# Kernel optimization log

Measured on AMD Instinct MI355X. Metric: run time of the kernel, lower is better.

The kernel has to match this reference:

```python
import jax, jax.numpy as jnp
import numpy as np

B, S, D = 2, 2048, 1024
E, K, DFF = 8, 2, 4 * 1024
EPS_GATE = 1e-8
EPS_LN = 1e-5


def setup_inputs() -> dict:
    key = jax.random.key(0)
    ks = jax.random.split(key, 4)
    scaled = lambda k, shape, fan: (jax.random.normal(k, shape, jnp.float32) / np.sqrt(fan).astype(np.float32))
    return {
        "x": jax.random.normal(ks[0], (B, S, D), jnp.float32),
        "Wg": scaled(ks[1], (D, E), D),
        "bg": jnp.zeros((E,), jnp.float32),
        "W1": scaled(ks[2], (E, D, DFF), D),
        "b1": jnp.zeros((E, DFF), jnp.float32),
        "W2": scaled(ks[3], (E, DFF, D), DFF),
        "b2": jnp.zeros((E, D), jnp.float32),
        "gamma": jnp.ones((D,), jnp.float32),
        "beta": jnp.zeros((D,), jnp.float32),
    }


def reference(x, Wg, bg, W1, b1, W2, b2, gamma, beta):
    b, s, d = x.shape
    xf = x.reshape(-1, d)                       # [T, D]
    T = xf.shape[0]
    num_experts = Wg.shape[1]

    # Gating: softmax over experts, top-k, renormalize selected weights.
    logits = xf @ Wg + bg                       # [T, E]
    w = jax.nn.softmax(logits, axis=-1)
    top_w, top_idx = jax.lax.top_k(w, K)        # [T, K]
    top_w = top_w / (top_w.sum(axis=-1, keepdims=True) + EPS_GATE)

    # Dense combine weights: cw[t, e] = renormalized weight if e selected else 0.
    cw = jnp.zeros((T, num_experts), xf.dtype).at[
        jnp.arange(T)[:, None], top_idx].add(top_w)

    # Expert FFNs (loop over small fixed expert count), weighted combine.
    out = jnp.zeros_like(xf)
    for e in range(num_experts):
        h = jax.nn.gelu(xf @ W1[e] + b1[e], approximate=False)  # [T, DFF]
        y = h @ W2[e] + b2[e]                                    # [T, D]
        out = out + cw[:, e:e + 1] * y

    # LayerNorm over the whole combined output (as in the torch module).
    mu = out.mean(axis=-1, keepdims=True)
    var = out.var(axis=-1, keepdims=True)
    out = (out - mu) / jnp.sqrt(var + EPS_LN) * gamma + beta
    return out.reshape(b, s, d)
```

## Files before the change

### kernel.cpp

```cpp
#include <hip/hip_runtime.h>
#include <hip/hip_bf16.h>

#define TOK  4096
#define DIMD 1024
#define NEXP 8
#define DFFN 4096
#define NSLOT   (TOK*2 + NEXP*128)
#define NRB128  ((TOK*2)/128 + NEXP)

typedef __attribute__((ext_vector_type(8))) short bf16x8;
typedef __attribute__((ext_vector_type(4))) float f32x4;

__device__ __forceinline__ unsigned short f2bf(float f){
  unsigned int u = __float_as_uint(f);
  unsigned int r = u + 0x7FFFu + ((u >> 16) & 1u);
  return (unsigned short)(r >> 16);
}

__device__ __forceinline__ float bf2f(unsigned short h){
  unsigned int u = ((unsigned int)h) << 16;
  return __uint_as_float(u);
}

__device__ __forceinline__ void gload_lds16(const void* g, void* l){
  __builtin_amdgcn_global_load_lds(
      (const __attribute__((address_space(1))) unsigned int*)g,
      (__attribute__((address_space(3))) unsigned int*)l, 16, 0, 0);
}

__global__ __launch_bounds__(256) void k_gate_trw1(
    const float* __restrict__ x, const float* __restrict__ Wg,
    const float* __restrict__ bg, int* __restrict__ topidx,
    float* __restrict__ topw, int* __restrict__ pos, int* __restrict__ count,
    unsigned short* __restrict__ xb,
    const float* __restrict__ W1, unsigned short* __restrict__ w1t)
{
  if (blockIdx.x < 2048){
    const int bid = blockIdx.x;
    const int e = bid >> 8, rem = bid & 255;
    const int R = DIMD, C = DFFN;
    const float* I = W1 + (size_t)e * R * C;
    unsigned short* O = w1t + (size_t)e * R * C;
    const int r0 = (rem >> 5) * 128, c0 = (rem & 31) * 128;
    __shared__ alignas(16) unsigned short tile[128*128];
    const int tid = threadIdx.x;
    const int qw = tid & 31;
    const int rw = tid >> 5;
    #pragma unroll
    for (int it = 0; it < 16; ++it){
      const int r = it * 8 + rw;
      const float4 v = *(const float4*)(I + (size_t)(r0 + r) * C + c0 + qw * 4);
      ushort4 o;
      o.x = f2bf(v.x); o.y = f2bf(v.y); o.z = f2bf(v.z); o.w = f2bf(v.w);
      const int slot = qw ^ ((r >> 2) & 31);
      *(ushort4*)&tile[r * 128 + slot * 4] = o;
    }
    __syncthreads();
    const int p  = tid & 31;
    const int cb = tid >> 5;
    #pragma unroll
    for (int it = 0; it < 4; ++it){
      const int cg = cb * 4 + it;
      const int sl = (cg ^ p) * 4;
      const ushort4 a0 = *(const ushort4*)&tile[(4*p + 0) * 128 + sl];
      const ushort4 a1 = *(const ushort4*)&tile[(4*p + 1) * 128 + sl];
      const ushort4 a2 = *(const ushort4*)&tile[(4*p + 2) * 128 + sl];
      const ushort4 a3 = *(const ushort4*)&tile[(4*p + 3) * 128 + sl];
      ushort4 o;
      o.x = a0.x; o.y = a1.x; o.z = a2.x; o.w = a3.x;
      *(ushort4*)(O + (size_t)(c0 + 4*cg + 0) * R + r0 + 4*p) = o;
      o.x = a0.y; o.y = a1.y; o.z = a2.y; o.w = a3.y;
      *(ushort4*)(O + (size_t)(c0 + 4*cg + 1) * R + r0 + 4*p) = o;
      o.x = a0.z; o.y = a1.z; o.z = a2.z; o.w = a3.z;
      *(ushort4*)(O + (size_t)(c0 + 4*cg + 2) * R + r0 + 4*p) = o;
      o.x = a0.w; o.y = a1.w; o.z = a2.w; o.w = a3.w;
      *(ushort4*)(O + (size_t)(c0 + 4*cg + 3) * R + r0 + 4*p) = o;
    }
    return;
  }
  const int gb = blockIdx.x - 2048;
  const int wid = threadIdx.x >> 6, lane = threadIdx.x & 63;
  const int t = gb * 4 + wid;
  const float* xr = x + (size_t)t * DIMD;
  unsigned short* xbr = xb + (size_t)t * DIMD;
  float acc[NEXP] = {0.f,0.f,0.f,0.f,0.f,0.f,0.f,0.f};
  #pragma unroll
  for (int j = 0; j < DIMD/64; ++j){
    const int d = j*64 + lane;
    const float xv = xr[d];
    xbr[d] = f2bf(xv);
    const float4 wa = *(const float4*)(Wg + (size_t)d*NEXP);
    const float4 wb = *(const float4*)(Wg + (size_t)d*NEXP + 4);
    acc[0] += xv*wa.x; acc[1] += xv*wa.y; acc[2] += xv*wa.z; acc[3] += xv*wa.w;
    acc[4] += xv*wb.x; acc[5] += xv*wb.y; acc[6] += xv*wb.z; acc[7] += xv*wb.w;
  }
  #pragma unroll
  for (int e = 0; e < NEXP; ++e){
    float v = acc[e];
    #pragma unroll
    for (int o = 32; o > 0; o >>= 1) v += __shfl_xor(v, o);
    acc[e] = v;
  }
  if (lane == 0){
    float lg[NEXP], m = -1e30f;
    #pragma unroll
    for (int e = 0; e < NEXP; ++e){ lg[e] = acc[e] + bg[e]; m = fmaxf(m, lg[e]); }
    float p[NEXP], S = 0.f;
    #pragma unroll
    for (int e = 0; e < NEXP; ++e){ p[e] = expf(lg[e] - m); S += p[e]; }
    int e0 = 0;
    #pragma unroll
    for (int e = 1; e < NEXP; ++e) if (p[e] > p[e0]) e0 = e;
    int e1 = (e0 == 0) ? 1 : 0;
    #pragma unroll
    for (int e = 0; e < NEXP; ++e){
      if (e == e0 || e == e1) continue;
      if (p[e] > p[e1]) e1 = e;
    }
    const float denom = p[e0] + p[e1] + 1e-8f * S;
    const float w0 = p[e0] / denom, w1 = p[e1] / denom;
    const int p0 = atomicAdd(&count[e0], 1);
    const int p1 = atomicAdd(&count[e1], 1);
    topidx[t*2] = e0; topidx[t*2+1] = e1;
    topw[t*2] = w0;   topw[t*2+1] = w1;
    pos[t*2] = p0;    pos[t*2+1] = p1;
  }
}

__global__ __launch_bounds__(256) void k_scatter(
    const int* __restrict__ topidx, const int* __restrict__ pos,
    const int* __restrict__ count, int* __restrict__ slot_of, int* __restrict__ tok_of)
{
  int basee[NEXP]; int bacc = 0;
  #pragma unroll
  for (int q = 0; q < NEXP; ++q){
    basee[q] = bacc << 7;
    bacc += (count[q] + 127) >> 7;
  }
  const int t = blockIdx.x * 256 + threadIdx.x;
  #pragma unroll
  for (int k = 0; k < 2; ++k){
    const int e = topidx[t*2+k];
    const int g = basee[e] + pos[t*2+k];
    slot_of[t*2+k] = g;
    tok_of[g] = t;
  }
}

template<int KD, int KSLICES, int NT, int MODE, int WAVES, int BM, int BN, int MINW, int TRW2>
__global__ __launch_bounds__(WAVES*64, MINW) void k_gemm(
    const unsigned short* __restrict__ A, const unsigned short* __restrict__ Bt,
    const float* __restrict__ bias, const int* __restrict__ tok_of,
    const int* __restrict__ count,
    unsigned short* __restrict__ outH, unsigned short* __restrict__ outY,
    unsigned short* __restrict__ outY1,
    const float* __restrict__ W2src, unsigned short* __restrict__ w2tdst)
{
  __shared__ alignas(16) unsigned short smem[BM*64 + BN*64];
  constexpr int CT = NT / BN;

  int by, ct, ks;
  if constexpr (TRW2 != 0){
    by = blockIdx.y;
    if (by >= NRB128){
      const int bid = (by - NRB128) * gridDim.x + blockIdx.x;
      const int eT = bid >> 8, rem = bid & 255;
      const int R = DFFN, C = DIMD;
      const float* I = W2src + (size_t)eT * R * C;
      unsigned short* O = w2tdst + (size_t)eT * R * C;
      const int r0 = (rem >> 3) * 128, c0 = (rem & 7) * 128;
      unsigned short* tile = smem;
      const int tid = threadIdx.x;
      const int qw = tid & 31, rw = tid >> 5;
      #pragma unroll
      for (int it = 0; it < 8; ++it){
        const int r = it * 16 + rw;
        const float4 v = *(const float4*)(I + (size_t)(r0 + r) * C + c0 + qw * 4);
        ushort4 o;
        o.x = f2bf(v.x); o.y = f2bf(v.y); o.z = f2bf(v.z); o.w = f2bf(v.w);
        const int slot = qw ^ ((r >> 2) & 31);
        *(ushort4*)&tile[r * 128 + slot * 4] = o;
      }
      __syncthreads();
      const int p = tid & 31, cb = tid >> 5;
      #pragma unroll
      for (int it = 0; it < 2; ++it){
        const int cg = cb * 2 + it;
        const int sl = (cg ^ p) * 4;
        const ushort4 a0 = *(const ushort4*)&tile[(4*p + 0) * 128 + sl];
        const ushort4 a1 = *(const ushort4*)&tile[(4*p + 1) * 128 + sl];
        const ushort4 a2 = *(const ushort4*)&tile[(4*p + 2) * 128 + sl];
        const ushort4 a3 = *(const ushort4*)&tile[(4*p + 3) * 128 + sl];
        ushort4 o;
        o.x = a0.x; o.y = a1.x; o.z = a2.x; o.w = a3.x;
        *(ushort4*)(O + (size_t)(c0 + 4*cg + 0) * R + r0 + 4*p) = o;
        o.x = a0.y; o.y = a1.y; o.z = a2.y; o.w = a3.y;
        *(ushort4*)(O + (size_t)(c0 + 4*cg + 1) * R + r0 + 4*p) = o;
        o.x = a0.z; o.y = a1.z; o.z = a2.z; o.w = a3.z;
        *(ushort4*)(O + (size_t)(c0 + 4*cg + 2) * R + r0 + 4*p) = o;
        o.x = a0.w; o.y = a1.w; o.z = a2.w; o.w = a3.w;
        *(ushort4*)(O + (size_t)(c0 + 4*cg + 3) * R + r0 + 4*p) = o;
      }
      return;
    }
    const int g = blockIdx.x + (int)gridDim.x * by;
    by = 9 * (g & 7) + ((g % 72) >> 3);
    ct = g / 72;
    ks = 0;
  } else {
    static_assert(CT * KSLICES == 8, "GEMM2 map assumes 8 blocks per rowblock");
    const int g = blockIdx.x;
    const int xx = g & 7;
    const int w  = g >> 3;
    by = 9 * xx + (w % 9);
    const int cw = w / 9;
    ct = cw % CT;
    ks = cw / CT;
  }

  int e = -1, b0 = 0;
  #pragma unroll
  for (int q = 0; q < NEXP; ++q){
    const int nb = (count[q] + 127) >> 7;
    if (e < 0){ if (by < b0 + nb) e = q; else b0 += nb; }
  }
  if (e < 0) return;
  constexpr int KSL = KD / KSLICES;
  const int kbase = ks * KSL;
  const int row0 = by * 128;
  constexpr int T   = WAVES * 64;
  constexpr int RA  = BM*8 / T;
  constexpr int RB  = BN*8 / T;
  constexpr int WN  = BN / 64;
  constexpr int WM  = WAVES / WN;
  constexpr int MR  = BM / WM / 16;
  unsigned short* sA = smem;
  unsigned short* sB = smem + BM*64;
  const int tid = threadIdx.x, wid = tid >> 6, lane = tid & 63;

  const unsigned short* aptr[RA];
  #pragma unroll
  for (int i = 0; i < RA; ++i){
    const int s = i*T + tid;
    const int row = s >> 3;
    const int c = (s & 7) ^ (row & 7);
    size_t arow;
    if (MODE == 1) arow = (size_t)tok_of[row0 + row] * KD;
    else           arow = (size_t)(row0 + row) * KD;
    aptr[i] = A + arow + kbase + c*8;
  }
  const unsigned short* bptr[RB];
  #pragma unroll
  for (int i = 0; i < RB; ++i){
    const int s = i*T + tid;
    const int row = s >> 3;
    const int c = (s & 7) ^ (row & 7);
    bptr[i] = Bt + ((size_t)e*NT + ct*BN + row) * KD + kbase + c*8;
  }

  f32x4 acc[MR][4] = {};
  const int wr = wid / WN, wc = wid % WN;

  int aoff[MR][2], boff[4][2];
  #pragma unroll
  for (int m = 0; m < MR; ++m){
    #pragma unroll
    for (int s = 0; s < 2; ++s){
      const int rowA = wr*(MR*16) + m*16 + (lane & 15);
      aoff[m][s] = rowA*64 + (((s*4) + (lane >> 4)) ^ (rowA & 7))*8;
    }
  }
  #pragma unroll
  for (int n = 0; n < 4; ++n){
    #pragma unroll
    for (int s = 0; s < 2; ++s){
      const int rowB = wc*64 + n*16 + (lane & 15);
      boff[n][s] = rowB*64 + (((s*4) + (lane >> 4)) ^ (rowB & 7))*8;
    }
  }

  for (int k0 = 0; k0 < KSL; k0 += 64){
    #pragma unroll
    for (int i = 0; i < RA; ++i)
      gload_lds16(aptr[i] + k0, &sA[(i*T + tid - lane)*8]);
    #pragma unroll
    for (int i = 0; i < RB; ++i)
      gload_lds16(bptr[i] + k0, &sB[(i*T + tid - lane)*8]);
    __syncthreads();
    #pragma unroll
    for (int s = 0; s < 2; ++s){
      bf16x8 af[MR], bfr[4];
      #pragma unroll
      for (int m = 0; m < MR; ++m) af[m] = *(const bf16x8*)&sA[aoff[m][s]];
      #pragma unroll
      for (int n = 0; n < 4; ++n) bfr[n] = *(const bf16x8*)&sB[boff[n][s]];
      #pragma unroll
      for (int m = 0; m < MR; ++m)
        #pragma unroll
        for (int n = 0; n < 4; ++n)
          acc[m][n] = __builtin_amdgcn_mfma_f32_16x16x32_bf16(af[m], bfr[n], acc[m][n], 0, 0, 0);
    }
    __syncthreads();
  }

  const float* be = bias + (size_t)e * NT;
  unsigned short* outYs = (ks == 0) ? outY : outY1;
  #pragma unroll
  for (int m = 0; m < MR; ++m){
    #pragma unroll
    for (int n = 0; n < 4; ++n){
      #pragma unroll
      for (int j = 0; j < 4; ++j){
        const int rl = wr*(MR*16) + m*16 + ((lane >> 4) << 2) + j;
        const int ng = ct*BN + wc*64 + n*16 + (lane & 15);
        const size_t orow = (size_t)(row0 + rl) * NT + ng;
        if (MODE == 1){
          const float u = acc[m][n][j] + be[ng];
          float y = 0.7978845608028654f * (u + 0.044715f * u * u * u);
          y = fminf(fmaxf(y, -15.f), 15.f);
          const float ex = __expf(2.f * y);
          const float th = (ex - 1.f) / (ex + 1.f);
          outH[orow] = f2bf(0.5f * u * (1.f + th));
        } else {
          outYs[orow] = f2bf(acc[m][n][j] + ((ks == 0) ? be[ng] : 0.f));
        }
      }
    }
  }
}

__global__ __launch_bounds__(256) void k_combine_ln(
    const unsigned short* __restrict__ Ys0, const unsigned short* __restrict__ Ys1,
    const int* __restrict__ slot_of,
    const float* __restrict__ topw, const float* __restrict__ gamma,
    const float* __restrict__ beta, float* __restrict__ out)
{
  const int t = blockIdx.x;
  const int g0 = slot_of[t*2], g1 = slot_of[t*2+1];
  const float w0 = topw[t*2], w1 = topw[t*2+1];
  const int c = threadIdx.x;
  const ushort4 a0 = *(const ushort4*)(Ys0 + (size_t)g0*DIMD + c*4);
  const ushort4 a1 = *(const ushort4*)(Ys1 + (size_t)g0*DIMD + c*4);
  const ushort4 b0 = *(const ushort4*)(Ys0 + (size_t)g1*DIMD + c*4);
  const ushort4 b1 = *(const ushort4*)(Ys1 + (size_t)g1*DIMD + c*4);
  float4 v;
  v.x = w0*(bf2f(a0.x)+bf2f(a1.x)) + w1*(bf2f(b0.x)+bf2f(b1.x));
  v.y = w0*(bf2f(a0.y)+bf2f(a1.y)) + w1*(bf2f(b0.y)+bf2f(b1.y));
  v.z = w0*(bf2f(a0.z)+bf2f(a1.z)) + w1*(bf2f(b0.z)+bf2f(b1.z));
  v.w = w0*(bf2f(a0.w)+bf2f(a1.w)) + w1*(bf2f(b0.w)+bf2f(b1.w));
  float s  = v.x + v.y + v.z + v.w;
  float ss = v.x*v.x + v.y*v.y + v.z*v.z + v.w*v.w;
  #pragma unroll
  for (int o = 32; o > 0; o >>= 1){ s += __shfl_xor(s, o); ss += __shfl_xor(ss, o); }
  __shared__ float red[8];
  const int wid = threadIdx.x >> 6, lane = threadIdx.x & 63;
  if (lane == 0){ red[wid] = s; red[4 + wid] = ss; }
  __syncthreads();
  const float S  = red[0] + red[1] + red[2] + red[3];
  const float SS = red[4] + red[5] + red[6] + red[7];
  const float mu  = S * (1.f/DIMD);
  const float var = SS * (1.f/DIMD) - mu*mu;
  const float inv = rsqrtf(var + 1e-5f);
  const float4 gm = *(const float4*)(gamma + c*4);
  const float4 bt = *(const float4*)(beta + c*4);
  float4 o;
  o.x = (v.x - mu)*inv*gm.x + bt.x;
  o.y = (v.y - mu)*inv*gm.y + bt.y;
  o.z = (v.z - mu)*inv*gm.z + bt.z;
  o.w = (v.w - mu)*inv*gm.w + bt.w;
  *(float4*)(out + (size_t)t*DIMD + c*4) = o;
}

extern "C" void kernel_launch(void* const* d_in, const int* in_sizes, int n_in,
                              void* d_out, int out_size, void* d_ws, size_t ws_size,
                              hipStream_t stream)
{
  const float* x     = (const float*)d_in[0];
  const float* Wg    = (const float*)d_in[1];
  const float* bg    = (const float*)d_in[2];
  const float* W1    = (const float*)d_in[3];
  const float* b1    = (const float*)d_in[4];
  const float* W2    = (const float*)d_in[5];
  const float* b2    = (const float*)d_in[6];
  const float* gamma = (const float*)d_in[7];
  const float* beta  = (const float*)d_in[8];
  float* out = (float*)d_out;

  char* ws = (char*)d_ws;
  size_t off = 0;
  auto alloc = [&](size_t b){ char* p = ws + off; off += (b + 255) & ~(size_t)255; return p; };
  unsigned short* xb  = (unsigned short*)alloc((size_t)TOK*DIMD*2);
  unsigned short* w1t = (unsigned short*)alloc((size_t)NEXP*DFFN*DIMD*2);
  unsigned short* w2t = (unsigned short*)alloc((size_t)NEXP*DIMD*DFFN*2);
  unsigned short* Hs  = (unsigned short*)alloc((size_t)NSLOT*DFFN*2);
  int*   topidx  = (int*)alloc(TOK*2*4);
  float* topw    = (float*)alloc(TOK*2*4);
  int*   pos     = (int*)alloc(TOK*2*4);
  int*   slot_of = (int*)alloc(TOK*2*4);
  int*   tok_of  = (int*)alloc(NSLOT*4);
  int*   count   = (int*)alloc(256);
  unsigned short* Ys0b = (unsigned short*)w1t;
  unsigned short* Ys1b = Ys0b + (size_t)NSLOT*DIMD;

  (void)hipMemsetAsync(count, 0, NEXP*sizeof(int), stream);
  (void)hipMemsetAsync(tok_of, 0, NSLOT*sizeof(int), stream);
  k_gate_trw1<<<3072, 256, 0, stream>>>(x, Wg, bg, topidx, topw, pos, count, xb, W1, w1t);
  k_scatter<<<TOK/256, 256, 0, stream>>>(topidx, pos, count, slot_of, tok_of);
  k_gemm<DIMD, 1, DFFN, 1, 8, 128, 256, 4, 1><<<dim3(DFFN/256, NRB128 + 128), 512, 0, stream>>>(
      xb, w1t, b1, tok_of, count, Hs, nullptr, nullptr, W2, w2t);
  k_gemm<DFFN, 2, DIMD, 2, 8, 128, 256, 4, 0><<<dim3((DIMD/256)*NRB128*2), 512, 0, stream>>>(
      Hs, w2t, b2, tok_of, count, nullptr, Ys0b, Ys1b, nullptr, nullptr);
  k_combine_ln<<<TOK, 256, 0, stream>>>(Ys0b, Ys1b, slot_of, topw, gamma, beta, out);
}
```

Measured before the change: 394.5 us.

## Fuse W1 fp32-to-bf16 conversion into first expert GEMM B-tile load

```diff
diff --git a/kernel.cpp b/kernel.cpp
--- a/kernel.cpp
+++ b/kernel.cpp
@@ -28,57 +28,13 @@
       (__attribute__((address_space(3))) unsigned int*)l, 16, 0, 0);
 }
 
-__global__ __launch_bounds__(256) void k_gate_trw1(
+__global__ __launch_bounds__(256) void k_gate(
     const float* __restrict__ x, const float* __restrict__ Wg,
     const float* __restrict__ bg, int* __restrict__ topidx,
     float* __restrict__ topw, int* __restrict__ pos, int* __restrict__ count,
-    unsigned short* __restrict__ xb,
-    const float* __restrict__ W1, unsigned short* __restrict__ w1t)
-{
-  if (blockIdx.x < 2048){
-    const int bid = blockIdx.x;
-    const int e = bid >> 8, rem = bid & 255;
-    const int R = DIMD, C = DFFN;
-    const float* I = W1 + (size_t)e * R * C;
-    unsigned short* O = w1t + (size_t)e * R * C;
-    const int r0 = (rem >> 5) * 128, c0 = (rem & 31) * 128;
-    __shared__ alignas(16) unsigned short tile[128*128];
-    const int tid = threadIdx.x;
-    const int qw = tid & 31;
-    const int rw = tid >> 5;
-    #pragma unroll
-    for (int it = 0; it < 16; ++it){
-      const int r = it * 8 + rw;
-      const float4 v = *(const float4*)(I + (size_t)(r0 + r) * C + c0 + qw * 4);
-      ushort4 o;
-      o.x = f2bf(v.x); o.y = f2bf(v.y); o.z = f2bf(v.z); o.w = f2bf(v.w);
-      const int slot = qw ^ ((r >> 2) & 31);
-      *(ushort4*)&tile[r * 128 + slot * 4] = o;
-    }
-    __syncthreads();
-    const int p  = tid & 31;
-    const int cb = tid >> 5;
-    #pragma unroll
-    for (int it = 0; it < 4; ++it){
-      const int cg = cb * 4 + it;
-      const int sl = (cg ^ p) * 4;
-      const ushort4 a0 = *(const ushort4*)&tile[(4*p + 0) * 128 + sl];
-      const ushort4 a1 = *(const ushort4*)&tile[(4*p + 1) * 128 + sl];
-      const ushort4 a2 = *(const ushort4*)&tile[(4*p + 2) * 128 + sl];
-      const ushort4 a3 = *(const ushort4*)&tile[(4*p + 3) * 128 + sl];
-      ushort4 o;
-      o.x = a0.x; o.y = a1.x; o.z = a2.x; o.w = a3.x;
-      *(ushort4*)(O + (size_t)(c0 + 4*cg + 0) * R + r0 + 4*p) = o;
-      o.x = a0.y; o.y = a1.y; o.z = a2.y; o.w = a3.y;
-      *(ushort4*)(O + (size_t)(c0 + 4*cg + 1) * R + r0 + 4*p) = o;
-      o.x = a0.z; o.y = a1.z; o.z = a2.z; o.w = a3.z;
-      *(ushort4*)(O + (size_t)(c0 + 4*cg + 2) * R + r0 + 4*p) = o;
-      o.x = a0.w; o.y = a1.w; o.z = a2.w; o.w = a3.w;
-      *(ushort4*)(O + (size_t)(c0 + 4*cg + 3) * R + r0 + 4*p) = o;
-    }
-    return;
-  }
-  const int gb = blockIdx.x - 2048;
+    unsigned short* __restrict__ xb)
+{
+  const int gb = blockIdx.x;
   const int wid = threadIdx.x >> 6, lane = threadIdx.x & 63;
   const int t = gb * 4 + wid;
   const float* xr = x + (size_t)t * DIMD;
@@ -147,14 +103,16 @@
   }
 }
 
-template<int KD, int KSLICES, int NT, int MODE, int WAVES, int BM, int BN, int MINW, int TRW2>
+template<int KD, int KSLICES, int NT, int MODE, int WAVES, int BM, int BN, int MINW,
+         int TRW2, int BF32>
 __global__ __launch_bounds__(WAVES*64, MINW) void k_gemm(
     const unsigned short* __restrict__ A, const unsigned short* __restrict__ Bt,
     const float* __restrict__ bias, const int* __restrict__ tok_of,
     const int* __restrict__ count,
     unsigned short* __restrict__ outH, unsigned short* __restrict__ outY,
     unsigned short* __restrict__ outY1,
-    const float* __restrict__ W2src, unsigned short* __restrict__ w2tdst)
+    const float* __restrict__ W2src, unsigned short* __restrict__ w2tdst,
+    const float* __restrict__ Bf32)
 {
   __shared__ alignas(16) unsigned short smem[BM*64 + BN*64];
   constexpr int CT = NT / BN;
@@ -250,13 +208,18 @@
     aptr[i] = A + arow + kbase + c*8;
   }
   const unsigned short* bptr[RB];
-  #pragma unroll
-  for (int i = 0; i < RB; ++i){
-    const int s = i*T + tid;
-    const int row = s >> 3;
-    const int c = (s & 7) ^ (row & 7);
-    bptr[i] = Bt + ((size_t)e*NT + ct*BN + row) * KD + kbase + c*8;
-  }
+  if constexpr (BF32 == 0){
+    #pragma unroll
+    for (int i = 0; i < RB; ++i){
+      const int s = i*T + tid;
+      const int row = s >> 3;
+      const int c = (s & 7) ^ (row & 7);
+      bptr[i] = Bt + ((size_t)e*NT + ct*BN + row) * KD + kbase + c*8;
+    }
+  }
+  const float* bfp = nullptr;
+  if constexpr (BF32 != 0)
+    bfp = Bf32 + ((size_t)e*KD + kbase + 8*wid) * NT + ct*BN + 4*lane;
 
   f32x4 acc[MR][4] = {};
   const int wr = wid / WN, wc = wid % WN;
@@ -280,12 +243,31 @@
   }
 
   for (int k0 = 0; k0 < KSL; k0 += 64){
-    #pragma unroll
-    for (int i = 0; i < RA; ++i)
-      gload_lds16(aptr[i] + k0, &sA[(i*T + tid - lane)*8]);
-    #pragma unroll
-    for (int i = 0; i < RB; ++i)
-      gload_lds16(bptr[i] + k0, &sB[(i*T + tid - lane)*8]);
+    if constexpr (BF32 != 0){
+      float4 bv[8];
+      const float* bp = bfp + (size_t)k0 * NT;
+      #pragma unroll
+      for (int r = 0; r < 8; ++r) bv[r] = *(const float4*)(bp + (size_t)r * NT);
+      #pragma unroll
+      for (int i = 0; i < RA; ++i)
+        gload_lds16(aptr[i] + k0, &sA[(i*T + tid - lane)*8]);
+      #pragma unroll
+      for (int j = 0; j < 4; ++j){
+        bf16x8 col;
+        #pragma unroll
+        for (int r = 0; r < 8; ++r)
+          col[r] = (short)f2bf(((const float*)&bv[r])[j]);
+        const int n = 4*lane + j;
+        *(bf16x8*)&sB[n*64 + ((wid ^ (n & 7)))*8] = col;
+      }
+    } else {
+      #pragma unroll
+      for (int i = 0; i < RA; ++i)
+        gload_lds16(aptr[i] + k0, &sA[(i*T + tid - lane)*8]);
+      #pragma unroll
+      for (int i = 0; i < RB; ++i)
+        gload_lds16(bptr[i] + k0, &sB[(i*T + tid - lane)*8]);
+    }
     __syncthreads();
     #pragma unroll
     for (int s = 0; s < 2; ++s){
@@ -390,7 +372,8 @@
   size_t off = 0;
   auto alloc = [&](size_t b){ char* p = ws + off; off += (b + 255) & ~(size_t)255; return p; };
   unsigned short* xb  = (unsigned short*)alloc((size_t)TOK*DIMD*2);
-  unsigned short* w1t = (unsigned short*)alloc((size_t)NEXP*DFFN*DIMD*2);
+  unsigned short* Ys0b = (unsigned short*)alloc((size_t)NSLOT*DIMD*2);
+  unsigned short* Ys1b = (unsigned short*)alloc((size_t)NSLOT*DIMD*2);
   unsigned short* w2t = (unsigned short*)alloc((size_t)NEXP*DIMD*DFFN*2);
   unsigned short* Hs  = (unsigned short*)alloc((size_t)NSLOT*DFFN*2);
   int*   topidx  = (int*)alloc(TOK*2*4);
@@ -399,16 +382,14 @@
   int*   slot_of = (int*)alloc(TOK*2*4);
   int*   tok_of  = (int*)alloc(NSLOT*4);
   int*   count   = (int*)alloc(256);
-  unsigned short* Ys0b = (unsigned short*)w1t;
-  unsigned short* Ys1b = Ys0b + (size_t)NSLOT*DIMD;
 
   (void)hipMemsetAsync(count, 0, NEXP*sizeof(int), stream);
   (void)hipMemsetAsync(tok_of, 0, NSLOT*sizeof(int), stream);
-  k_gate_trw1<<<3072, 256, 0, stream>>>(x, Wg, bg, topidx, topw, pos, count, xb, W1, w1t);
+  k_gate<<<TOK/4, 256, 0, stream>>>(x, Wg, bg, topidx, topw, pos, count, xb);
   k_scatter<<<TOK/256, 256, 0, stream>>>(topidx, pos, count, slot_of, tok_of);
-  k_gemm<DIMD, 1, DFFN, 1, 8, 128, 256, 4, 1><<<dim3(DFFN/256, NRB128 + 128), 512, 0, stream>>>(
-      xb, w1t, b1, tok_of, count, Hs, nullptr, nullptr, W2, w2t);
-  k_gemm<DFFN, 2, DIMD, 2, 8, 128, 256, 4, 0><<<dim3((DIMD/256)*NRB128*2), 512, 0, stream>>>(
-      Hs, w2t, b2, tok_of, count, nullptr, Ys0b, Ys1b, nullptr, nullptr);
+  k_gemm<DIMD, 1, DFFN, 1, 8, 128, 256, 3, 1, 1><<<dim3(DFFN/256, NRB128 + 128), 512, 0, stream>>>(
+      xb, nullptr, b1, tok_of, count, Hs, nullptr, nullptr, W2, w2t, W1);
+  k_gemm<DFFN, 2, DIMD, 2, 8, 128, 256, 4, 0, 0><<<dim3((DIMD/256)*NRB128*2), 512, 0, stream>>>(
+      Hs, w2t, b2, tok_of, count, nullptr, Ys0b, Ys1b, nullptr, nullptr, nullptr);
   k_combine_ln<<<TOK, 256, 0, stream>>>(Ys0b, Ys1b, slot_of, topw, gamma, beta, out);
 }
```

Result: slower. 414.6 us (+5.1%).
